# Kernel optimization log

Measured on AMD Instinct MI355X. Metric: run time of the kernel, lower is better.

The kernel has to match this reference:

```python
import jax, jax.numpy as jnp
import numpy as np

B = 65536            # batch of configurations
F = 32               # num_frames (joints)
DOF = 29             # controllable joints
# tree: chain 0..29, two mimic branches off frame 10; parent index always < child -> topo order = range(F)
PARENTS = [-1] + list(range(29)) + [10, 10]


def _np_rodrigues(w):
    th = np.linalg.norm(w)
    if th < 1e-12:
        return np.eye(3)
    k = w / th
    K = np.array([[0, -k[2], k[1]], [k[2], 0, -k[0]], [-k[1], k[0], 0]])
    return np.eye(3) + np.sin(th) * K + (1 - np.cos(th)) * (K @ K)


def setup_inputs() -> dict:
    key = jax.random.key(0)
    rng = np.random.default_rng(0)
    # joint types: 0 fixed, 1 revolute, 2 prismatic
    types = np.ones(F, dtype=np.int32)
    types[0] = 0
    types[15] = 2
    types[22] = 2
    # controllable = non-fixed, non-mimic (mimic dst = 30, 31)
    ctrl = np.array([i for i in range(F) if types[i] != 0 and i not in (30, 31)], dtype=np.int32)
    assert ctrl.shape[0] == DOF
    axes = rng.normal(size=(F, 3)).astype(np.float32)
    axes /= np.linalg.norm(axes, axis=-1, keepdims=True)
    origins = np.tile(np.eye(4, dtype=np.float32), (F, 1, 1))
    for i in range(F):
        origins[i, :3, :3] = _np_rodrigues(rng.normal(size=3) * 0.5)
        origins[i, :3, 3] = rng.normal(size=3) * 0.1
    joint_angles = jax.random.normal(key, (B, DOF), dtype=jnp.float32)
    return {
        "joint_angles": joint_angles,
        "all_axes": jnp.asarray(axes),
        "all_origins": jnp.asarray(origins),
        "mimic_multipliers": jnp.array([1.0, -1.0], dtype=jnp.float32),
        "mimic_offsets": jnp.array([0.1, -0.1], dtype=jnp.float32),
        "ctrlable_indices": jnp.asarray(ctrl),
        "mimic_src_indices": jnp.array([5, 6], dtype=jnp.int32),
        "mimic_dst_indices": jnp.array([30, 31], dtype=jnp.int32),
        "joint_types": jnp.asarray(types),
    }


def exp_map(w):
    # axis-angle (...,3) -> rotation (...,3,3), Rodrigues, eps-safe at w=0
    theta = jnp.sqrt(jnp.sum(w * w, axis=-1, keepdims=True) + 1e-18)  # (...,1)
    k = w / theta
    kx, ky, kz = k[..., 0], k[..., 1], k[..., 2]
    zero = jnp.zeros_like(kx)
    K = jnp.stack(
        [jnp.stack([zero, -kz, ky], -1),
         jnp.stack([kz, zero, -kx], -1),
         jnp.stack([-ky, kx, zero], -1)], -2)
    st = jnp.sin(theta)[..., None]
    ct = jnp.cos(theta)[..., None]
    return jnp.eye(3, dtype=w.dtype) + st * K + (1.0 - ct) * (K @ K)


def _fk(joint_angles, all_axes, all_origins, mimic_multipliers, mimic_offsets,
        ctrlable_indices, mimic_src_indices, mimic_dst_indices, joint_types):
    b = joint_angles.shape[0]
    # scatter controllable angles, then mimic gather/scatter
    all_angles = jnp.zeros((b, F), joint_angles.dtype).at[:, ctrlable_indices].set(joint_angles)
    mimic_vals = all_angles[:, mimic_src_indices] * mimic_multipliers + mimic_offsets
    all_angles = all_angles.at[:, mimic_dst_indices].set(mimic_vals)
    # per-frame local motion (B,F,4,4)
    w = all_axes[None, :, :] * all_angles[..., None]          # (B,F,3)
    R = exp_map(w)                                            # (B,F,3,3)
    R = jnp.where((joint_types == 1)[None, :, None, None], R, jnp.eye(3, dtype=w.dtype))
    t = jnp.where((joint_types == 2)[None, :, None], w, jnp.zeros((), w.dtype))
    top = jnp.concatenate([R, t[..., None]], axis=-1)         # (B,F,3,4)
    bottom = jnp.broadcast_to(jnp.array([0, 0, 0, 1], w.dtype), (b, F, 1, 4))
    motion = jnp.concatenate([top, bottom], axis=-2)          # (B,F,4,4)
    local = jnp.einsum('fij,bfjk->bfik', all_origins, motion)
    # sequential tree-structured compose (F is small & static -> unrolled)
    poses = []
    for i in range(F):
        p = PARENTS[i]
        li = local[:, i]
        poses.append(li if p < 0 else poses[p] @ li)
    return jnp.stack(poses, axis=1)                            # (B,F,4,4)


def reference(joint_angles, all_axes, all_origins, mimic_multipliers, mimic_offsets,
              ctrlable_indices, mimic_src_indices, mimic_dst_indices, joint_types):
    return _fk(joint_angles, all_axes, all_origins, mimic_multipliers, mimic_offsets,
               ctrlable_indices, mimic_src_indices, mimic_dst_indices, joint_types)
```

## Files before the change

kernel.cpp:

```cpp
#include <hip/hip_runtime.h>
#include <math.h>

#define BLOCK 256
#define NF 32
#define NDOF 29
#define ANG_STRIDE 257
#define OUT_STRIDE_F4 9

__global__ __launch_bounds__(BLOCK) void fk_kernel(
    const float* __restrict__ ja,
    const float* __restrict__ axes,
    const float* __restrict__ origins,
    const float* __restrict__ mmul,
    const float* __restrict__ moff,
    const int*   __restrict__ ctrl,
    const int*   __restrict__ msrc,
    const int*   __restrict__ mdst,
    const int*   __restrict__ types,
    float*       __restrict__ out,
    int B)
{
    __shared__ float s_ax[NF][3];
    __shared__ float s_or[NF][12];
    __shared__ int   s_type[NF];
    __shared__ int   s_slot[NF];
    __shared__ float s_mult[NF];
    __shared__ float s_off[NF];
    __shared__ float s_ang[NDOF * ANG_STRIDE];
    __shared__ float4 s_out[BLOCK * OUT_STRIDE_F4];

    const int tid = threadIdx.x;

    if (tid < NF) {
        const int f = tid;
        s_ax[f][0] = axes[f*3+0];
        s_ax[f][1] = axes[f*3+1];
        s_ax[f][2] = axes[f*3+2];
        #pragma unroll
        for (int r = 0; r < 3; ++r)
            #pragma unroll
            for (int c = 0; c < 4; ++c)
                s_or[f][r*4+c] = origins[f*16 + r*4 + c];
        s_type[f] = types[f];
        int slot = -1;
        for (int j = 0; j < NDOF; ++j) if (ctrl[j] == f) slot = j;
        float mu = 1.0f, of = 0.0f;
        for (int m = 0; m < 2; ++m) {
            if (mdst[m] == f) {
                const int sf = msrc[m];
                for (int j = 0; j < NDOF; ++j) if (ctrl[j] == sf) slot = j;
                mu = mmul[m]; of = moff[m];
            }
        }
        s_slot[f] = slot; s_mult[f] = mu; s_off[f] = of;
    }

    const long blk0 = (long)blockIdx.x * BLOCK;
    {
        const long base = blk0 * NDOF;
        const long lim  = (long)B * NDOF;
        for (int i = tid; i < BLOCK * NDOF; i += BLOCK) {
            const long g = base + i;
            const int slot = i % NDOF;
            const int brel = i / NDOF;
            s_ang[slot * ANG_STRIDE + brel] = (g < lim) ? ja[g] : 0.0f;
        }
    }
    __syncthreads();

    float Pr[9], Pt[3];
    float Qr[9], Qt[3];

    auto compute_local = [&](int f, float* Lr, float* Lt) {
        const int   slot = s_slot[f];
        const float a = (slot >= 0)
            ? fmaf(s_mult[f], s_ang[slot * ANG_STRIDE + tid], s_off[f]) : 0.0f;
        const float wx = a * s_ax[f][0];
        const float wy = a * s_ax[f][1];
        const float wz = a * s_ax[f][2];
        const int ty = s_type[f];
        float R0,R1,R2,R3,R4,R5,R6,R7,R8;
        if (ty == 1) {
            const float t2 = wx*wx + wy*wy + wz*wz;
            const float th = sqrtf(t2 + 1e-18f);
            const float inv = 1.0f / th;
            const float kx = wx*inv, ky = wy*inv, kz = wz*inv;
            float s, c;
            __sincosf(th, &s, &c);
            const float v = 1.0f - c;
            R0 = fmaf(v*kx, kx, c);
            R1 = v*kx*ky - s*kz;
            R2 = v*kx*kz + s*ky;
            R3 = v*kx*ky + s*kz;
            R4 = fmaf(v*ky, ky, c);
            R5 = v*ky*kz - s*kx;
            R6 = v*kx*kz - s*ky;
            R7 = v*ky*kz + s*kx;
            R8 = fmaf(v*kz, kz, c);
        } else {
            R0=1.f;R1=0.f;R2=0.f;R3=0.f;R4=1.f;R5=0.f;R6=0.f;R7=0.f;R8=1.f;
        }
        float tx, tyv, tz;
        if (ty == 2) { tx = wx; tyv = wy; tz = wz; }
        else         { tx = 0.f; tyv = 0.f; tz = 0.f; }
        const float* O = s_or[f];
        #pragma unroll
        for (int r = 0; r < 3; ++r) {
            const float o0 = O[r*4+0], o1 = O[r*4+1], o2 = O[r*4+2], o3 = O[r*4+3];
            Lr[r*3+0] = o0*R0 + o1*R3 + o2*R6;
            Lr[r*3+1] = o0*R1 + o1*R4 + o2*R7;
            Lr[r*3+2] = o0*R2 + o1*R5 + o2*R8;
            Lt[r]     = o0*tx + o1*tyv + o2*tz + o3;
        }
    };

    float4* const out4 = (float4*)out;

    #pragma unroll 1
    for (int c = 0; c < 16; ++c) {
        const int f0 = 2 * c;
        #pragma unroll
        for (int lf = 0; lf < 2; ++lf) {
            const int f = f0 + lf;
            float Lr[9], Lt[3];
            compute_local(f, Lr, Lt);
            float Wr[9], Wt[3];
            if (f == 0) {
                #pragma unroll
                for (int i = 0; i < 9; ++i) Wr[i] = Lr[i];
                Wt[0]=Lt[0]; Wt[1]=Lt[1]; Wt[2]=Lt[2];
            } else if (f <= 29) {
                #pragma unroll
                for (int r = 0; r < 3; ++r) {
                    const float p0 = Pr[r*3+0], p1 = Pr[r*3+1], p2 = Pr[r*3+2];
                    Wr[r*3+0] = p0*Lr[0] + p1*Lr[3] + p2*Lr[6];
                    Wr[r*3+1] = p0*Lr[1] + p1*Lr[4] + p2*Lr[7];
                    Wr[r*3+2] = p0*Lr[2] + p1*Lr[5] + p2*Lr[8];
                    Wt[r]     = p0*Lt[0] + p1*Lt[1] + p2*Lt[2] + Pt[r];
                }
            } else {
                #pragma unroll
                for (int r = 0; r < 3; ++r) {
                    const float p0 = Qr[r*3+0], p1 = Qr[r*3+1], p2 = Qr[r*3+2];
                    Wr[r*3+0] = p0*Lr[0] + p1*Lr[3] + p2*Lr[6];
                    Wr[r*3+1] = p0*Lr[1] + p1*Lr[4] + p2*Lr[7];
                    Wr[r*3+2] = p0*Lr[2] + p1*Lr[5] + p2*Lr[8];
                    Wt[r]     = p0*Lt[0] + p1*Lt[1] + p2*Lt[2] + Qt[r];
                }
            }
            if (f <= 29) {
                #pragma unroll
                for (int i = 0; i < 9; ++i) Pr[i] = Wr[i];
                Pt[0]=Wt[0]; Pt[1]=Wt[1]; Pt[2]=Wt[2];
                if (f == 10) {
                    #pragma unroll
                    for (int i = 0; i < 9; ++i) Qr[i] = Pr[i];
                    Qt[0]=Pt[0]; Qt[1]=Pt[1]; Qt[2]=Pt[2];
                }
            }
            float4* slot4 = &s_out[tid * OUT_STRIDE_F4 + lf * 4];
            slot4[0] = make_float4(Wr[0], Wr[1], Wr[2], Wt[0]);
            slot4[1] = make_float4(Wr[3], Wr[4], Wr[5], Wt[1]);
            slot4[2] = make_float4(Wr[6], Wr[7], Wr[8], Wt[2]);
            slot4[3] = make_float4(0.0f, 0.0f, 0.0f, 1.0f);
        }
        __syncthreads();
        #pragma unroll
        for (int k = 0; k < 8; ++k) {
            const int i = tid + k * BLOCK;
            const int brel = i >> 3;
            const int q    = i & 7;
            const long bb  = blk0 + brel;
            if (bb < (long)B)
                out4[bb * 128 + f0 * 4 + q] = s_out[brel * OUT_STRIDE_F4 + q];
        }
        __syncthreads();
    }
}

extern "C" void kernel_launch(void* const* d_in, const int* in_sizes, int n_in,
                              void* d_out, int out_size, void* d_ws, size_t ws_size,
                              hipStream_t stream) {
    const float* ja   = (const float*)d_in[0];
    const float* axes = (const float*)d_in[1];
    const float* orig = (const float*)d_in[2];
    const float* mmul = (const float*)d_in[3];
    const float* moff = (const float*)d_in[4];
    const int*   ctrl = (const int*)d_in[5];
    const int*   msrc = (const int*)d_in[6];
    const int*   mdst = (const int*)d_in[7];
    const int*   typs = (const int*)d_in[8];
    float* out = (float*)d_out;

    const int B = in_sizes[0] / NDOF;
    const int grid = (B + BLOCK - 1) / BLOCK;
    fk_kernel<<<grid, BLOCK, 0, stream>>>(ja, axes, orig, mmul, moff,
                                          ctrl, msrc, mdst, typs, out, B);
}
```

Baseline: 170.6 us.

## Use single-wave blocks with double-buffered LDS staging and wave barriers

Shrinks the block to one 64-lane wavefront so the output staging can use wave-level barriers instead of block-wide __syncthreads, and stores one frame per iteration into a double-buffered LDS slot. The angle load and output store loops are restructured to match. Each output store now writes 64 contiguous bytes per batch element per frame instead of 128. The smaller block gives finer scheduling, but means more blocks and a less coalesced store pattern. Relying on wave_barrier alone for LDS ordering may be fragile.

```diff
diff --git a/kernel.cpp b/kernel.cpp
--- a/kernel.cpp
+++ b/kernel.cpp
@@ -1,11 +1,10 @@
 #include <hip/hip_runtime.h>
 #include <math.h>
 
-#define BLOCK 256
+#define BLOCK 64
 #define NF 32
 #define NDOF 29
-#define ANG_STRIDE 257
-#define OUT_STRIDE_F4 9
+#define SLOT_F4 5
 
 __global__ __launch_bounds__(BLOCK) void fk_kernel(
     const float* __restrict__ ja,
@@ -26,13 +25,13 @@
     __shared__ int   s_slot[NF];
     __shared__ float s_mult[NF];
     __shared__ float s_off[NF];
-    __shared__ float s_ang[NDOF * ANG_STRIDE];
-    __shared__ float4 s_out[BLOCK * OUT_STRIDE_F4];
+    __shared__ float s_ang[NDOF][BLOCK];
+    __shared__ float4 s_out[2][BLOCK * SLOT_F4];
 
-    const int tid = threadIdx.x;
+    const int lane = threadIdx.x;
 
-    if (tid < NF) {
-        const int f = tid;
+    if (lane < NF) {
+        const int f = lane;
         s_ax[f][0] = axes[f*3+0];
         s_ax[f][1] = axes[f*3+1];
         s_ax[f][2] = axes[f*3+2];
@@ -59,11 +58,11 @@
     {
         const long base = blk0 * NDOF;
         const long lim  = (long)B * NDOF;
-        for (int i = tid; i < BLOCK * NDOF; i += BLOCK) {
+        #pragma unroll 1
+        for (int k = 0; k < NDOF; ++k) {
+            const int  i = k * BLOCK + lane;
             const long g = base + i;
-            const int slot = i % NDOF;
-            const int brel = i / NDOF;
-            s_ang[slot * ANG_STRIDE + brel] = (g < lim) ? ja[g] : 0.0f;
+            s_ang[i % NDOF][i / NDOF] = (g < lim) ? ja[g] : 0.0f;
         }
     }
     __syncthreads();
@@ -71,10 +70,13 @@
     float Pr[9], Pt[3];
     float Qr[9], Qt[3];
 
-    auto compute_local = [&](int f, float* Lr, float* Lt) {
+    float4* const out4 = (float4*)out;
+    const long lim_b = (long)B;
+
+    #pragma unroll 1
+    for (int f = 0; f < NF; ++f) {
         const int   slot = s_slot[f];
-        const float a = (slot >= 0)
-            ? fmaf(s_mult[f], s_ang[slot * ANG_STRIDE + tid], s_off[f]) : 0.0f;
+        const float a = (slot >= 0) ? fmaf(s_mult[f], s_ang[slot][lane], s_off[f]) : 0.0f;
         const float wx = a * s_ax[f][0];
         const float wy = a * s_ax[f][1];
         const float wz = a * s_ax[f][2];
@@ -103,6 +105,8 @@
         float tx, tyv, tz;
         if (ty == 2) { tx = wx; tyv = wy; tz = wz; }
         else         { tx = 0.f; tyv = 0.f; tz = 0.f; }
+
+        float Lr[9], Lt[3];
         const float* O = s_or[f];
         #pragma unroll
         for (int r = 0; r < 3; ++r) {
@@ -112,69 +116,54 @@
             Lr[r*3+2] = o0*R2 + o1*R5 + o2*R8;
             Lt[r]     = o0*tx + o1*tyv + o2*tz + o3;
         }
-    };
 
-    float4* const out4 = (float4*)out;
+        float Wr[9], Wt[3];
+        if (f == 0) {
+            #pragma unroll
+            for (int i = 0; i < 9; ++i) Wr[i] = Lr[i];
+            Wt[0]=Lt[0]; Wt[1]=Lt[1]; Wt[2]=Lt[2];
+        } else {
+            const float* PR = (f >= 30) ? Qr : Pr;
+            const float* PT = (f >= 30) ? Qt : Pt;
+            #pragma unroll
+            for (int r = 0; r < 3; ++r) {
+                const float p0 = PR[r*3+0], p1 = PR[r*3+1], p2 = PR[r*3+2];
+                Wr[r*3+0] = p0*Lr[0] + p1*Lr[3] + p2*Lr[6];
+                Wr[r*3+1] = p0*Lr[1] + p1*Lr[4] + p2*Lr[7];
+                Wr[r*3+2] = p0*Lr[2] + p1*Lr[5] + p2*Lr[8];
+                Wt[r]     = p0*Lt[0] + p1*Lt[1] + p2*Lt[2] + PT[r];
+            }
+        }
+        if (f <= 29) {
+            #pragma unroll
+            for (int i = 0; i < 9; ++i) Pr[i] = Wr[i];
+            Pt[0]=Wt[0]; Pt[1]=Wt[1]; Pt[2]=Wt[2];
+            if (f == 10) {
+                #pragma unroll
+                for (int i = 0; i < 9; ++i) Qr[i] = Pr[i];
+                Qt[0]=Pt[0]; Qt[1]=Pt[1]; Qt[2]=Pt[2];
+            }
+        }
 
-    #pragma unroll 1
-    for (int c = 0; c < 16; ++c) {
-        const int f0 = 2 * c;
-        #pragma unroll
-        for (int lf = 0; lf < 2; ++lf) {
-            const int f = f0 + lf;
-            float Lr[9], Lt[3];
-            compute_local(f, Lr, Lt);
-            float Wr[9], Wt[3];
-            if (f == 0) {
-                #pragma unroll
-                for (int i = 0; i < 9; ++i) Wr[i] = Lr[i];
-                Wt[0]=Lt[0]; Wt[1]=Lt[1]; Wt[2]=Lt[2];
-            } else if (f <= 29) {
-                #pragma unroll
-                for (int r = 0; r < 3; ++r) {
-                    const float p0 = Pr[r*3+0], p1 = Pr[r*3+1], p2 = Pr[r*3+2];
-                    Wr[r*3+0] = p0*Lr[0] + p1*Lr[3] + p2*Lr[6];
-                    Wr[r*3+1] = p0*Lr[1] + p1*Lr[4] + p2*Lr[7];
-                    Wr[r*3+2] = p0*Lr[2] + p1*Lr[5] + p2*Lr[8];
-                    Wt[r]     = p0*Lt[0] + p1*Lt[1] + p2*Lt[2] + Pt[r];
-                }
-            } else {
-                #pragma unroll
-                for (int r = 0; r < 3; ++r) {
-                    const float p0 = Qr[r*3+0], p1 = Qr[r*3+1], p2 = Qr[r*3+2];
-                    Wr[r*3+0] = p0*Lr[0] + p1*Lr[3] + p2*Lr[6];
-                    Wr[r*3+1] = p0*Lr[1] + p1*Lr[4] + p2*Lr[7];
-                    Wr[r*3+2] = p0*Lr[2] + p1*Lr[5] + p2*Lr[8];
-                    Wt[r]     = p0*Lt[0] + p1*Lt[1] + p2*Lt[2] + Qt[r];
-                }
-            }
-            if (f <= 29) {
-                #pragma unroll
-                for (int i = 0; i < 9; ++i) Pr[i] = Wr[i];
-                Pt[0]=Wt[0]; Pt[1]=Wt[1]; Pt[2]=Wt[2];
-                if (f == 10) {
-                    #pragma unroll
-                    for (int i = 0; i < 9; ++i) Qr[i] = Pr[i];
-                    Qt[0]=Pt[0]; Qt[1]=Pt[1]; Qt[2]=Pt[2];
-                }
-            }
-            float4* slot4 = &s_out[tid * OUT_STRIDE_F4 + lf * 4];
+        float4* const buf = s_out[f & 1];
+        {
+            float4* slot4 = &buf[lane * SLOT_F4];
             slot4[0] = make_float4(Wr[0], Wr[1], Wr[2], Wt[0]);
             slot4[1] = make_float4(Wr[3], Wr[4], Wr[5], Wt[1]);
             slot4[2] = make_float4(Wr[6], Wr[7], Wr[8], Wt[2]);
             slot4[3] = make_float4(0.0f, 0.0f, 0.0f, 1.0f);
         }
-        __syncthreads();
+        __builtin_amdgcn_wave_barrier();
+        const int q  = lane & 3;
+        const int b0 = lane >> 2;
         #pragma unroll
-        for (int k = 0; k < 8; ++k) {
-            const int i = tid + k * BLOCK;
-            const int brel = i >> 3;
-            const int q    = i & 7;
-            const long bb  = blk0 + brel;
-            if (bb < (long)B)
-                out4[bb * 128 + f0 * 4 + q] = s_out[brel * OUT_STRIDE_F4 + q];
+        for (int k = 0; k < 4; ++k) {
+            const int  b  = b0 + 16 * k;
+            const long bb = blk0 + b;
+            if (bb < lim_b)
+                out4[bb * 128 + f * 4 + q] = buf[b * SLOT_F4 + q];
         }
-        __syncthreads();
+        __builtin_amdgcn_wave_barrier();
     }
 }
 
```

Result: no change. 170.7 us (+0.1%).
